# Kernel optimization log

Measured on AMD Instinct MI355X. Metric: run time of the kernel, lower is better.

Reference implementation:

```python
import jax, jax.numpy as jnp
import numpy as np

EPS = 1e-12  # matches NTMNet epsilon


def setup_inputs() -> dict:
    key = jax.random.key(0)
    ks = jax.random.split(key, 12)
    B, L, C, D, H = 64, 16384, 64, 256, 100
    F = D + 1 * C  # inputs concat flattened reading (1 reader)
    def w(k, shape):
        return jax.random.normal(k, shape, dtype=jnp.float32) * 0.05
    return {
        "inputs": w(ks[0], (B, D)),
        "reading": w(ks[1], (B, 1, C)),
        "memory": w(ks[2], (B, L, C)),
        "W1": w(ks[3], (F, H)), "b1": jnp.zeros((H,), jnp.float32),
        "W2": w(ks[4], (H, H)), "b2": jnp.zeros((H,), jnp.float32),
        "Wk_r": w(ks[5], (H, C)), "bk_r": jnp.zeros((C,), jnp.float32),
        "Ws_r": w(ks[6], (H, 1)), "bs_r": jnp.zeros((1,), jnp.float32),
        "Wk_w": w(ks[7], (H, C)), "bk_w": jnp.zeros((C,), jnp.float32),
        "Ws_w": w(ks[8], (H, 1)), "bs_w": jnp.zeros((1,), jnp.float32),
        "We": w(ks[9], (H, C)), "be": jnp.zeros((C,), jnp.float32),
        "Wa": w(ks[10], (H, C)), "ba": jnp.zeros((C,), jnp.float32),
    }


def reference(inputs, reading, memory, W1, b1, W2, b2,
              Wk_r, bk_r, Ws_r, bs_r, Wk_w, bk_w, Ws_w, bs_w,
              We, be, Wa, ba):
    B = inputs.shape[0]
    feat = jnp.concatenate([inputs, reading.reshape(B, -1)], axis=-1)
    h = jnp.tanh(jnp.tanh(feat @ W1 + b1) @ W2 + b2)  # [B,H]

    # memory normalized over the whole (lines, cols) matrix per batch element
    mnorm = jnp.sqrt(jnp.sum(memory * memory, axis=(-2, -1), keepdims=True))
    mem_n = memory / jnp.maximum(mnorm, EPS)  # [B,L,C]

    def addressing(Wk, bk, Ws, bs):
        # content addressing: cosine-sim of key vs memory rows, sharpened softmax
        kvec = h @ Wk + bk  # [B,C] (no activation)
        kvec = kvec / jnp.maximum(jnp.linalg.norm(kvec, axis=1, keepdims=True), EPS)
        s = jax.nn.sigmoid(h @ Ws + bs)  # [B,1] strength
        K = jnp.einsum('blc,bc->bl', mem_n, kvec)  # [B,L]
        return jax.nn.softmax(K * s, axis=-1)  # [B,L]

    # read head
    w_r = addressing(Wk_r, bk_r, Ws_r, bs_r)
    read = jnp.einsum('bl,blc->bc', w_r, memory)  # [B,C]

    # write head: erase then add
    w_w = addressing(Wk_w, bk_w, Ws_w, bs_w)
    e = jax.nn.sigmoid(h @ We + be)  # [B,C]
    a = jax.nn.sigmoid(h @ Wa + ba)  # [B,C]
    ww = w_w[:, :, None]  # [B,L,1]
    new_mem = memory * (1.0 - ww * e[:, None, :]) + ww * a[:, None, :]  # [B,L,C]
    return read, new_mem
```

## Files before the change

### kernel.cpp

```cpp
#include <hip/hip_runtime.h>
#include <math.h>

#define B 64
#define L 16384
#define C 64
#define D 256
#define H 100
#define F 320
#define EPSV 1e-12f

typedef float nfloat4 __attribute__((ext_vector_type(4)));

__device__ inline float waveReduceSum(float v) {
    v += __shfl_xor(v, 32);
    v += __shfl_xor(v, 16);
    v += __shfl_xor(v, 8);
    v += __shfl_xor(v, 4);
    v += __shfl_xor(v, 2);
    v += __shfl_xor(v, 1);
    return v;
}

__global__ __launch_bounds__(128) void head_kernel(
    const float* __restrict__ inputs, const float* __restrict__ reading,
    const float* __restrict__ W1, const float* __restrict__ b1,
    const float* __restrict__ W2, const float* __restrict__ b2,
    const float* __restrict__ Wk_r, const float* __restrict__ bk_r,
    const float* __restrict__ Ws_r, const float* __restrict__ bs_r,
    const float* __restrict__ Wk_w, const float* __restrict__ bk_w,
    const float* __restrict__ Ws_w, const float* __restrict__ bs_w,
    const float* __restrict__ We, const float* __restrict__ be,
    const float* __restrict__ Wa, const float* __restrict__ ba,
    float* __restrict__ kv_r, float* __restrict__ kv_w,
    float* __restrict__ ev, float* __restrict__ av,
    float* __restrict__ s_r, float* __restrict__ s_w)
{
    const int b = blockIdx.x;
    const int t = threadIdx.x;
    __shared__ float feat[F];
    __shared__ float h1[H];
    __shared__ float h2[H];
    __shared__ float kr[C], kw[C], ee[C], aa[C];
    __shared__ float inv_r, inv_w;

    for (int i = t; i < D; i += 128) feat[i] = inputs[b * D + i];
    if (t < C) feat[D + t] = reading[b * C + t];
    __syncthreads();

    if (t < H) {
        float acc = b1[t];
        for (int f = 0; f < F; ++f) acc += feat[f] * W1[f * H + t];
        h1[t] = tanhf(acc);
    }
    __syncthreads();
    if (t < H) {
        float acc = b2[t];
        for (int k = 0; k < H; ++k) acc += h1[k] * W2[k * H + t];
        h2[t] = tanhf(acc);
    }
    __syncthreads();

    if (t < C) {
        float a0 = bk_r[t], a1 = bk_w[t], a2 = be[t], a3 = ba[t];
        for (int j = 0; j < H; ++j) {
            float hv = h2[j];
            a0 += hv * Wk_r[j * C + t];
            a1 += hv * Wk_w[j * C + t];
            a2 += hv * We[j * C + t];
            a3 += hv * Wa[j * C + t];
        }
        kr[t] = a0; kw[t] = a1;
        ee[t] = 1.f / (1.f + expf(-a2));
        aa[t] = 1.f / (1.f + expf(-a3));
    } else if (t == 64 || t == 65) {
        const float* Ws = (t == 64) ? Ws_r : Ws_w;
        float acc = (t == 64) ? bs_r[0] : bs_w[0];
        for (int j = 0; j < H; ++j) acc += h2[j] * Ws[j];
        float s = 1.f / (1.f + expf(-acc));
        if (t == 64) s_r[b] = s; else s_w[b] = s;
    }
    __syncthreads();
    if (t < 64) {
        const float xr = kr[t], xw = kw[t];
        const float nr = waveReduceSum(xr * xr);
        const float nw = waveReduceSum(xw * xw);
        if (t == 0) {
            inv_r = 1.f / fmaxf(sqrtf(nr), EPSV);
            inv_w = 1.f / fmaxf(sqrtf(nw), EPSV);
        }
    }
    __syncthreads();
    if (t < C) {
        kv_r[b * C + t] = kr[t] * inv_r;
        kv_w[b * C + t] = kw[t] * inv_w;
        ev[b * C + t] = ee[t];
        av[b * C + t] = aa[t];
    }
}

__global__ __launch_bounds__(256) void passA_kernel(
    const float* __restrict__ mem,
    const float* __restrict__ kv_r, const float* __restrict__ kv_w,
    float2* __restrict__ dot2,
    float* __restrict__ sumsq)
{
    const int b = blockIdx.y;
    const int t = threadIdx.x;
    const int wave = t >> 6, lane = t & 63;
    const int sub = lane >> 4, m = lane & 15;

    const float4 kr = *(const float4*)(kv_r + b * C + m * 4);
    const float4 kw = *(const float4*)(kv_w + b * C + m * 4);
    const float4* memv = (const float4*)(mem + (size_t)b * L * C);
    float2* d2 = dot2 + (size_t)b * L;

    float lss = 0.f;
    const int row0 = blockIdx.x * 512;
    #pragma unroll 4
    for (int it = 0; it < 32; ++it) {
        const int row = row0 + it * 16 + wave * 4 + sub;
        const float4 v = memv[row * 16 + m];
        float pr = v.x * kr.x + v.y * kr.y + v.z * kr.z + v.w * kr.w;
        float pw = v.x * kw.x + v.y * kw.y + v.z * kw.z + v.w * kw.w;
        lss += v.x * v.x + v.y * v.y + v.z * v.z + v.w * v.w;
        pr += __shfl_xor(pr, 1);
        pw += __shfl_xor(pw, 1);
        float x = (m & 1) ? pw : pr;
        x += __shfl_xor(x, 2);
        x += __shfl_xor(x, 4);
        x += __shfl_xor(x, 8);
        const float y = __shfl_xor(x, 1);
        if (m == 0) d2[row] = make_float2(x, y);
    }
    lss = waveReduceSum(lss);
    __shared__ float wsum[4];
    if (lane == 0) wsum[wave] = lss;
    __syncthreads();
    if (t == 0) atomicAdd(&sumsq[b], wsum[0] + wsum[1] + wsum[2] + wsum[3]);
}

__global__ __launch_bounds__(1024) void stats_kernel(
    const float2* __restrict__ dot2,
    const float* __restrict__ s_r, const float* __restrict__ s_w,
    const float* __restrict__ sumsq,
    float* __restrict__ stats)
{
    const int b = blockIdx.x;
    const int t = threadIdx.x;
    const int wave = t >> 6, lane = t & 63;
    const float invn = 1.f / fmaxf(sqrtf(sumsq[b]), EPSV);
    const float sc_r = s_r[b] * invn;
    const float sc_w = s_w[b] * invn;
    const float2* p = dot2 + (size_t)b * L;

    float2 v[16];
    #pragma unroll
    for (int k = 0; k < 16; ++k) v[k] = p[t + k * 1024];

    float mr = -INFINITY, mw = -INFINITY;
    #pragma unroll
    for (int k = 0; k < 16; ++k) {
        mr = fmaxf(mr, v[k].x * sc_r);
        mw = fmaxf(mw, v[k].y * sc_w);
    }
    #pragma unroll
    for (int off = 32; off; off >>= 1) {
        mr = fmaxf(mr, __shfl_xor(mr, off));
        mw = fmaxf(mw, __shfl_xor(mw, off));
    }
    __shared__ float redr[16], redw[16];
    if (lane == 0) { redr[wave] = mr; redw[wave] = mw; }
    __syncthreads();
    if (t == 0) {
        float a = redr[0], c = redw[0];
        for (int i = 1; i < 16; ++i) { a = fmaxf(a, redr[i]); c = fmaxf(c, redw[i]); }
        redr[0] = a; redw[0] = c;
    }
    __syncthreads();
    const float bmr = redr[0], bmw = redw[0];
    __syncthreads();

    float sr = 0.f, sw = 0.f;
    #pragma unroll
    for (int k = 0; k < 16; ++k) {
        sr += expf(v[k].x * sc_r - bmr);
        sw += expf(v[k].y * sc_w - bmw);
    }
    sr = waveReduceSum(sr);
    sw = waveReduceSum(sw);
    if (lane == 0) { redr[wave] = sr; redw[wave] = sw; }
    __syncthreads();
    if (t == 0) {
        float a = 0.f, c = 0.f;
        for (int i = 0; i < 16; ++i) { a += redr[i]; c += redw[i]; }
        float* st = stats + b * 8;
        st[0] = sc_r; st[1] = bmr; st[2] = 1.f / a;
        st[3] = sc_w; st[4] = bmw; st[5] = 1.f / c;
    }
}

__global__ __launch_bounds__(256) void passB_kernel(
    const float* __restrict__ mem,
    const float2* __restrict__ dot2,
    const float* __restrict__ stats,
    const float* __restrict__ ev, const float* __restrict__ av,
    float* __restrict__ out_read, float* __restrict__ new_mem)
{
    const int b = blockIdx.y;
    const int t = threadIdx.x;
    const int wave = t >> 6, lane = t & 63;
    const int sub = lane >> 4, m = lane & 15;

    const float4 e4 = *(const float4*)(ev + b * C + m * 4);
    const float4 a4 = *(const float4*)(av + b * C + m * 4);
    const float* st = stats + b * 8;
    const float sc_r = st[0], mx_r = st[1], inv_r = st[2];
    const float sc_w = st[3], mx_w = st[4], inv_w = st[5];
    const float4* memv = (const float4*)(mem + (size_t)b * L * C);
    nfloat4* outv = (nfloat4*)(new_mem + (size_t)b * L * C);
    const float2* d2 = dot2 + (size_t)b * L;

    float4 racc = {0.f, 0.f, 0.f, 0.f};
    const int row0 = blockIdx.x * 512;
    #pragma unroll 2
    for (int it = 0; it < 32; ++it) {
        const int row = row0 + it * 16 + wave * 4 + sub;
        const float2 d = d2[row];
        const float wr = expf(d.x * sc_r - mx_r) * inv_r;
        const float ww = expf(d.y * sc_w - mx_w) * inv_w;
        const float4 v = memv[row * 16 + m];
        nfloat4 nm;
        nm.x = v.x * (1.f - ww * e4.x) + ww * a4.x;
        nm.y = v.y * (1.f - ww * e4.y) + ww * a4.y;
        nm.z = v.z * (1.f - ww * e4.z) + ww * a4.z;
        nm.w = v.w * (1.f - ww * e4.w) + ww * a4.w;
        __builtin_nontemporal_store(nm, &outv[row * 16 + m]);
        racc.x += wr * v.x; racc.y += wr * v.y;
        racc.z += wr * v.z; racc.w += wr * v.w;
    }
    racc.x += __shfl_xor(racc.x, 16); racc.x += __shfl_xor(racc.x, 32);
    racc.y += __shfl_xor(racc.y, 16); racc.y += __shfl_xor(racc.y, 32);
    racc.z += __shfl_xor(racc.z, 16); racc.z += __shfl_xor(racc.z, 32);
    racc.w += __shfl_xor(racc.w, 16); racc.w += __shfl_xor(racc.w, 32);
    __shared__ float lds[4][64];
    if (lane < 16) {
        lds[wave][m * 4 + 0] = racc.x;
        lds[wave][m * 4 + 1] = racc.y;
        lds[wave][m * 4 + 2] = racc.z;
        lds[wave][m * 4 + 3] = racc.w;
    }
    __syncthreads();
    if (t < 64) {
        float tot = lds[0][t] + lds[1][t] + lds[2][t] + lds[3][t];
        atomicAdd(&out_read[b * C + t], tot);
    }
}

extern "C" void kernel_launch(void* const* d_in, const int* in_sizes, int n_in,
                              void* d_out, int out_size, void* d_ws, size_t ws_size,
                              hipStream_t stream) {
    const float* inputs  = (const float*)d_in[0];
    const float* reading = (const float*)d_in[1];
    const float* memory  = (const float*)d_in[2];
    const float* W1 = (const float*)d_in[3];
    const float* b1 = (const float*)d_in[4];
    const float* W2 = (const float*)d_in[5];
    const float* b2 = (const float*)d_in[6];
    const float* Wk_r = (const float*)d_in[7];
    const float* bk_r = (const float*)d_in[8];
    const float* Ws_r = (const float*)d_in[9];
    const float* bs_r = (const float*)d_in[10];
    const float* Wk_w = (const float*)d_in[11];
    const float* bk_w = (const float*)d_in[12];
    const float* Ws_w = (const float*)d_in[13];
    const float* bs_w = (const float*)d_in[14];
    const float* We = (const float*)d_in[15];
    const float* be = (const float*)d_in[16];
    const float* Wa = (const float*)d_in[17];
    const float* ba = (const float*)d_in[18];

    float* ws = (float*)d_ws;
    float* kv_r  = ws;
    float* kv_w  = ws + 4096;
    float* ev    = ws + 8192;
    float* av    = ws + 12288;
    float* s_r   = ws + 16384;
    float* s_w   = ws + 16448;
    float* sumsq = ws + 16512;
    float* stats = ws + 16576;
    float* dot2f = ws + 17408;

    float* out = (float*)d_out;
    float* out_read = out;
    float* new_mem  = out + 4096;

    hipMemsetAsync(sumsq, 0, B * sizeof(float), stream);
    hipMemsetAsync(out_read, 0, B * C * sizeof(float), stream);

    head_kernel<<<B, 128, 0, stream>>>(
        inputs, reading, W1, b1, W2, b2, Wk_r, bk_r, Ws_r, bs_r,
        Wk_w, bk_w, Ws_w, bs_w, We, be, Wa, ba,
        kv_r, kv_w, ev, av, s_r, s_w);

    passA_kernel<<<dim3(32, B), 256, 0, stream>>>(
        memory, kv_r, kv_w, (float2*)dot2f, sumsq);

    stats_kernel<<<B, 1024, 0, stream>>>(
        (const float2*)dot2f, s_r, s_w, sumsq, stats);

    passB_kernel<<<dim3(32, B), 256, 0, stream>>>(
        memory, (const float2*)dot2f, stats, ev, av, out_read, new_mem);
}
```

Before: 570.7 us.

## Fuse all four stages into one cooperative persistent kernel with grid syncs

```diff
diff --git a/kernel.cpp b/kernel.cpp
--- a/kernel.cpp
+++ b/kernel.cpp
@@ -1,5 +1,8 @@
 #include <hip/hip_runtime.h>
+#include <hip/hip_cooperative_groups.h>
 #include <math.h>
+
+namespace cg = cooperative_groups;
 
 #define B 64
 #define L 16384
@@ -8,6 +11,8 @@
 #define H 100
 #define F 320
 #define EPSV 1e-12f
+#define MAXBLK 1024
+#define RPB 1024
 
 typedef float nfloat4 __attribute__((ext_vector_type(4)));
 
@@ -19,6 +24,234 @@
     v += __shfl_xor(v, 2);
     v += __shfl_xor(v, 1);
     return v;
+}
+
+__device__ inline void grid_sync_coherent(cg::grid_group& grid) {
+    __threadfence();
+    grid.sync();
+    __threadfence();
+}
+
+__global__ __launch_bounds__(256, 4) void fused_kernel(
+    const float* __restrict__ inputs, const float* __restrict__ reading,
+    const float* __restrict__ mem,
+    const float* __restrict__ W1, const float* __restrict__ b1,
+    const float* __restrict__ W2, const float* __restrict__ b2,
+    const float* __restrict__ Wk_r, const float* __restrict__ bk_r,
+    const float* __restrict__ Ws_r, const float* __restrict__ bs_r,
+    const float* __restrict__ Wk_w, const float* __restrict__ bk_w,
+    const float* __restrict__ Ws_w, const float* __restrict__ bs_w,
+    const float* __restrict__ We, const float* __restrict__ be,
+    const float* __restrict__ Wa, const float* __restrict__ ba,
+    float* __restrict__ kv_r, float* __restrict__ kv_w,
+    float* __restrict__ ev, float* __restrict__ av,
+    float* __restrict__ s_r, float* __restrict__ s_w,
+    float* __restrict__ sumsq, float* __restrict__ stats,
+    float2* __restrict__ dot2,
+    float* __restrict__ out_read, float* __restrict__ new_mem)
+{
+    cg::grid_group grid = cg::this_grid();
+    const int g = blockIdx.x;
+    const int nb = gridDim.x;
+    const int t = threadIdx.x;
+    const int wave = t >> 6, lane = t & 63;
+    const int sub = lane >> 4, m = lane & 15;
+
+    __shared__ float feat[F];
+    __shared__ float h1[H], h2[H];
+    __shared__ float kr_s[C], kw_s[C], ee_s[C], aa_s[C];
+    __shared__ float invs[2];
+    __shared__ float red0[4], red1[4];
+    __shared__ float lds4[4][C];
+
+    for (int u = g; u < 2 * B; u += nb) {
+        if (u < B) {
+            const int b = u;
+            feat[t] = inputs[b * D + t];
+            if (t < C) feat[D + t] = reading[b * C + t];
+            __syncthreads();
+            if (t < H) {
+                float acc = b1[t];
+                for (int f = 0; f < F; ++f) acc += feat[f] * W1[f * H + t];
+                h1[t] = tanhf(acc);
+            }
+            __syncthreads();
+            if (t < H) {
+                float acc = b2[t];
+                for (int k = 0; k < H; ++k) acc += h1[k] * W2[k * H + t];
+                h2[t] = tanhf(acc);
+            }
+            __syncthreads();
+            if (t < C) {
+                float a0 = bk_r[t], a1 = bk_w[t], a2 = be[t], a3 = ba[t];
+                for (int j = 0; j < H; ++j) {
+                    const float hv = h2[j];
+                    a0 += hv * Wk_r[j * C + t];
+                    a1 += hv * Wk_w[j * C + t];
+                    a2 += hv * We[j * C + t];
+                    a3 += hv * Wa[j * C + t];
+                }
+                kr_s[t] = a0; kw_s[t] = a1;
+                ee_s[t] = 1.f / (1.f + expf(-a2));
+                aa_s[t] = 1.f / (1.f + expf(-a3));
+            } else if (t == 64 || t == 65) {
+                const float* Ws = (t == 64) ? Ws_r : Ws_w;
+                float acc = (t == 64) ? bs_r[0] : bs_w[0];
+                for (int j = 0; j < H; ++j) acc += h2[j] * Ws[j];
+                const float s = 1.f / (1.f + expf(-acc));
+                if (t == 64) s_r[b] = s; else s_w[b] = s;
+            }
+            __syncthreads();
+            if (t < 64) {
+                const float xr = kr_s[t], xw = kw_s[t];
+                const float nr = waveReduceSum(xr * xr);
+                const float nw = waveReduceSum(xw * xw);
+                if (t == 0) {
+                    invs[0] = 1.f / fmaxf(sqrtf(nr), EPSV);
+                    invs[1] = 1.f / fmaxf(sqrtf(nw), EPSV);
+                }
+            }
+            __syncthreads();
+            if (t < C) {
+                kv_r[b * C + t] = kr_s[t] * invs[0];
+                kv_w[b * C + t] = kw_s[t] * invs[1];
+                ev[b * C + t] = ee_s[t];
+                av[b * C + t] = aa_s[t];
+            }
+            __syncthreads();
+        } else {
+            const int b = u - B;
+            if (t < C) out_read[b * C + t] = 0.f;
+            if (t == 64) sumsq[b] = 0.f;
+        }
+    }
+    grid_sync_coherent(grid);
+
+    for (int u = g; u < B * 16; u += nb) {
+        const int b = u >> 4;
+        const int chunk = u & 15;
+        const float4 kr = *(const float4*)(kv_r + b * C + m * 4);
+        const float4 kw = *(const float4*)(kv_w + b * C + m * 4);
+        const float4* memv = (const float4*)(mem + (size_t)b * L * C);
+        float2* d2 = dot2 + (size_t)b * L;
+        float lss = 0.f;
+        const int row0 = chunk * RPB;
+        #pragma unroll 4
+        for (int it = 0; it < 64; ++it) {
+            const int row = row0 + it * 16 + wave * 4 + sub;
+            const float4 v = memv[row * 16 + m];
+            float pr = v.x * kr.x + v.y * kr.y + v.z * kr.z + v.w * kr.w;
+            float pw = v.x * kw.x + v.y * kw.y + v.z * kw.z + v.w * kw.w;
+            lss += v.x * v.x + v.y * v.y + v.z * v.z + v.w * v.w;
+            pr += __shfl_xor(pr, 1);
+            pw += __shfl_xor(pw, 1);
+            float x = (m & 1) ? pw : pr;
+            x += __shfl_xor(x, 2);
+            x += __shfl_xor(x, 4);
+            x += __shfl_xor(x, 8);
+            const float y = __shfl_xor(x, 1);
+            if (m == 0) d2[row] = make_float2(x, y);
+        }
+        lss = waveReduceSum(lss);
+        if (lane == 0) red0[wave] = lss;
+        __syncthreads();
+        if (t == 0) atomicAdd(&sumsq[b], red0[0] + red0[1] + red0[2] + red0[3]);
+        __syncthreads();
+    }
+    grid_sync_coherent(grid);
+
+    for (int u = g; u < B; u += nb) {
+        const int b = u;
+        const float invn = 1.f / fmaxf(sqrtf(sumsq[b]), EPSV);
+        const float sc_r = s_r[b] * invn;
+        const float sc_w = s_w[b] * invn;
+        const float2* p = dot2 + (size_t)b * L;
+
+        float mr = -INFINITY, mw = -INFINITY;
+        for (int i = t; i < L; i += 256) {
+            const float2 d = p[i];
+            mr = fmaxf(mr, d.x * sc_r);
+            mw = fmaxf(mw, d.y * sc_w);
+        }
+        #pragma unroll
+        for (int off = 32; off; off >>= 1) {
+            mr = fmaxf(mr, __shfl_xor(mr, off));
+            mw = fmaxf(mw, __shfl_xor(mw, off));
+        }
+        __syncthreads();
+        if (lane == 0) { red0[wave] = mr; red1[wave] = mw; }
+        __syncthreads();
+        const float bmr = fmaxf(fmaxf(red0[0], red0[1]), fmaxf(red0[2], red0[3]));
+        const float bmw = fmaxf(fmaxf(red1[0], red1[1]), fmaxf(red1[2], red1[3]));
+
+        float sr = 0.f, sw = 0.f;
+        for (int i = t; i < L; i += 256) {
+            const float2 d = p[i];
+            sr += expf(d.x * sc_r - bmr);
+            sw += expf(d.y * sc_w - bmw);
+        }
+        sr = waveReduceSum(sr);
+        sw = waveReduceSum(sw);
+        __syncthreads();
+        if (lane == 0) { red0[wave] = sr; red1[wave] = sw; }
+        __syncthreads();
+        if (t == 0) {
+            float* st = stats + b * 8;
+            st[0] = sc_r; st[1] = bmr; st[2] = 1.f / (red0[0] + red0[1] + red0[2] + red0[3]);
+            st[3] = sc_w; st[4] = bmw; st[5] = 1.f / (red1[0] + red1[1] + red1[2] + red1[3]);
+        }
+        __syncthreads();
+    }
+    grid_sync_coherent(grid);
+
+    for (int u = g; u < B * 16; u += nb) {
+        const int b = u >> 4;
+        const int chunk = u & 15;
+        const float4 e4 = *(const float4*)(ev + b * C + m * 4);
+        const float4 a4 = *(const float4*)(av + b * C + m * 4);
+        const float* st = stats + b * 8;
+        const float sc_r = st[0], mx_r = st[1], inv_r = st[2];
+        const float sc_w = st[3], mx_w = st[4], inv_w = st[5];
+        const float4* memv = (const float4*)(mem + (size_t)b * L * C);
+        nfloat4* outv = (nfloat4*)(new_mem + (size_t)b * L * C);
+        const float2* d2 = dot2 + (size_t)b * L;
+
+        float4 racc = {0.f, 0.f, 0.f, 0.f};
+        const int row0 = chunk * RPB;
+        #pragma unroll 2
+        for (int it = 0; it < 64; ++it) {
+            const int row = row0 + it * 16 + wave * 4 + sub;
+            const float2 d = d2[row];
+            const float wr = expf(d.x * sc_r - mx_r) * inv_r;
+            const float ww = expf(d.y * sc_w - mx_w) * inv_w;
+            const float4 v = memv[row * 16 + m];
+            nfloat4 nm;
+            nm.x = v.x * (1.f - ww * e4.x) + ww * a4.x;
+            nm.y = v.y * (1.f - ww * e4.y) + ww * a4.y;
+            nm.z = v.z * (1.f - ww * e4.z) + ww * a4.z;
+            nm.w = v.w * (1.f - ww * e4.w) + ww * a4.w;
+            __builtin_nontemporal_store(nm, &outv[row * 16 + m]);
+            racc.x += wr * v.x; racc.y += wr * v.y;
+            racc.z += wr * v.z; racc.w += wr * v.w;
+        }
+        racc.x += __shfl_xor(racc.x, 16); racc.x += __shfl_xor(racc.x, 32);
+        racc.y += __shfl_xor(racc.y, 16); racc.y += __shfl_xor(racc.y, 32);
+        racc.z += __shfl_xor(racc.z, 16); racc.z += __shfl_xor(racc.z, 32);
+        racc.w += __shfl_xor(racc.w, 16); racc.w += __shfl_xor(racc.w, 32);
+        __syncthreads();
+        if (lane < 16) {
+            lds4[wave][m * 4 + 0] = racc.x;
+            lds4[wave][m * 4 + 1] = racc.y;
+            lds4[wave][m * 4 + 2] = racc.z;
+            lds4[wave][m * 4 + 3] = racc.w;
+        }
+        __syncthreads();
+        if (t < 64) {
+            const float tot = lds4[0][t] + lds4[1][t] + lds4[2][t] + lds4[3][t];
+            atomicAdd(&out_read[b * C + t], tot);
+        }
+        __syncthreads();
+    }
 }
 
 __global__ __launch_bounds__(128) void head_kernel(
@@ -288,14 +521,50 @@
     float* s_w   = ws + 16448;
     float* sumsq = ws + 16512;
     float* stats = ws + 16576;
-    float* dot2f = ws + 17408;
+    float2* dot2 = (float2*)(ws + 17408);
 
     float* out = (float*)d_out;
     float* out_read = out;
     float* new_mem  = out + 4096;
 
-    hipMemsetAsync(sumsq, 0, B * sizeof(float), stream);
-    hipMemsetAsync(out_read, 0, B * C * sizeof(float), stream);
+    static int coop_blocks = -2;
+    if (coop_blocks == -2) {
+        int dev = 0;
+        (void)hipGetDevice(&dev);
+        int supports = 0;
+        (void)hipDeviceGetAttribute(&supports, hipDeviceAttributeCooperativeLaunch, dev);
+        int numCU = 0;
+        (void)hipDeviceGetAttribute(&numCU, hipDeviceAttributeMultiprocessorCount, dev);
+        int perCU = 0;
+        hipError_t oe = hipOccupancyMaxActiveBlocksPerMultiprocessor(
+            &perCU, (const void*)fused_kernel, 256, 0);
+        if (supports && oe == hipSuccess && perCU > 0 && numCU > 0) {
+            long total = (long)perCU * (long)numCU;
+            coop_blocks = (int)(total > MAXBLK ? MAXBLK : total);
+        } else {
+            coop_blocks = -1;
+        }
+    }
+
+    if (coop_blocks > 0) {
+        void* args[] = {
+            (void*)&inputs, (void*)&reading, (void*)&memory,
+            (void*)&W1, (void*)&b1, (void*)&W2, (void*)&b2,
+            (void*)&Wk_r, (void*)&bk_r, (void*)&Ws_r, (void*)&bs_r,
+            (void*)&Wk_w, (void*)&bk_w, (void*)&Ws_w, (void*)&bs_w,
+            (void*)&We, (void*)&be, (void*)&Wa, (void*)&ba,
+            (void*)&kv_r, (void*)&kv_w, (void*)&ev, (void*)&av,
+            (void*)&s_r, (void*)&s_w, (void*)&sumsq, (void*)&stats,
+            (void*)&dot2, (void*)&out_read, (void*)&new_mem
+        };
+        hipError_t err = hipLaunchCooperativeKernel(
+            (void*)fused_kernel, dim3(coop_blocks), dim3(256), args, 0, stream);
+        if (err == hipSuccess) return;
+        coop_blocks = -1;
+    }
+
+    (void)hipMemsetAsync(sumsq, 0, B * sizeof(float), stream);
+    (void)hipMemsetAsync(out_read, 0, B * C * sizeof(float), stream);
 
     head_kernel<<<B, 128, 0, stream>>>(
         inputs, reading, W1, b1, W2, b2, Wk_r, bk_r, Ws_r, bs_r,
@@ -303,11 +572,11 @@
         kv_r, kv_w, ev, av, s_r, s_w);
 
     passA_kernel<<<dim3(32, B), 256, 0, stream>>>(
-        memory, kv_r, kv_w, (float2*)dot2f, sumsq);
+        memory, kv_r, kv_w, dot2, sumsq);
 
     stats_kernel<<<B, 1024, 0, stream>>>(
-        (const float2*)dot2f, s_r, s_w, sumsq, stats);
+        dot2, s_r, s_w, sumsq, stats);
 
     passB_kernel<<<dim3(32, B), 256, 0, stream>>>(
-        memory, (const float2*)dot2f, stats, ev, av, out_read, new_mem);
-}
+        memory, dot2, stats, ev, av, out_read, new_mem);
+}
```

Result: slower. 1.009 ms (+76.9%).

## Drop softmax max pass and dot buffer by recomputing dots across three memory passes

Applied to the files above, without the earlier changes.

```diff
diff --git a/kernel.cpp b/kernel.cpp
--- a/kernel.cpp
+++ b/kernel.cpp
@@ -8,6 +8,8 @@
 #define H 100
 #define F 320
 #define EPSV 1e-12f
+#define CHUNKS 32
+#define RPC 512
 
 typedef float nfloat4 __attribute__((ext_vector_type(4)));
 
@@ -21,8 +23,9 @@
     return v;
 }
 
-__global__ __launch_bounds__(128) void head_kernel(
+__global__ __launch_bounds__(256) void k1_kernel(
     const float* __restrict__ inputs, const float* __restrict__ reading,
+    const float* __restrict__ mem,
     const float* __restrict__ W1, const float* __restrict__ b1,
     const float* __restrict__ W2, const float* __restrict__ b2,
     const float* __restrict__ Wk_r, const float* __restrict__ bk_r,
@@ -33,96 +36,131 @@
     const float* __restrict__ Wa, const float* __restrict__ ba,
     float* __restrict__ kv_r, float* __restrict__ kv_w,
     float* __restrict__ ev, float* __restrict__ av,
-    float* __restrict__ s_r, float* __restrict__ s_w)
+    float* __restrict__ s_r, float* __restrict__ s_w,
+    float* __restrict__ partial_ss)
 {
-    const int b = blockIdx.x;
+    const int g = blockIdx.x;
     const int t = threadIdx.x;
-    __shared__ float feat[F];
-    __shared__ float h1[H];
-    __shared__ float h2[H];
-    __shared__ float kr[C], kw[C], ee[C], aa[C];
-    __shared__ float inv_r, inv_w;
-
-    for (int i = t; i < D; i += 128) feat[i] = inputs[b * D + i];
-    if (t < C) feat[D + t] = reading[b * C + t];
-    __syncthreads();
-
-    if (t < H) {
-        float acc = b1[t];
-        for (int f = 0; f < F; ++f) acc += feat[f] * W1[f * H + t];
-        h1[t] = tanhf(acc);
-    }
-    __syncthreads();
-    if (t < H) {
-        float acc = b2[t];
-        for (int k = 0; k < H; ++k) acc += h1[k] * W2[k * H + t];
-        h2[t] = tanhf(acc);
-    }
-    __syncthreads();
-
-    if (t < C) {
-        float a0 = bk_r[t], a1 = bk_w[t], a2 = be[t], a3 = ba[t];
-        for (int j = 0; j < H; ++j) {
-            float hv = h2[j];
-            a0 += hv * Wk_r[j * C + t];
-            a1 += hv * Wk_w[j * C + t];
-            a2 += hv * We[j * C + t];
-            a3 += hv * Wa[j * C + t];
-        }
-        kr[t] = a0; kw[t] = a1;
-        ee[t] = 1.f / (1.f + expf(-a2));
-        aa[t] = 1.f / (1.f + expf(-a3));
-    } else if (t == 64 || t == 65) {
-        const float* Ws = (t == 64) ? Ws_r : Ws_w;
-        float acc = (t == 64) ? bs_r[0] : bs_w[0];
-        for (int j = 0; j < H; ++j) acc += h2[j] * Ws[j];
-        float s = 1.f / (1.f + expf(-acc));
-        if (t == 64) s_r[b] = s; else s_w[b] = s;
-    }
-    __syncthreads();
-    if (t < 64) {
-        const float xr = kr[t], xw = kw[t];
-        const float nr = waveReduceSum(xr * xr);
-        const float nw = waveReduceSum(xw * xw);
-        if (t == 0) {
-            inv_r = 1.f / fmaxf(sqrtf(nr), EPSV);
-            inv_w = 1.f / fmaxf(sqrtf(nw), EPSV);
-        }
-    }
-    __syncthreads();
-    if (t < C) {
-        kv_r[b * C + t] = kr[t] * inv_r;
-        kv_w[b * C + t] = kw[t] * inv_w;
-        ev[b * C + t] = ee[t];
-        av[b * C + t] = aa[t];
-    }
-}
-
-__global__ __launch_bounds__(256) void passA_kernel(
+
+    if (g < B * CHUNKS) {
+        const int b = g >> 5, chunk = g & 31;
+        const int wave = t >> 6, lane = t & 63;
+        const int sub = lane >> 4, m = lane & 15;
+        const float4* memv = (const float4*)(mem + (size_t)b * L * C);
+        float lss = 0.f;
+        const int row0 = chunk * RPC;
+        #pragma unroll 8
+        for (int it = 0; it < 32; ++it) {
+            const int row = row0 + it * 16 + wave * 4 + sub;
+            const float4 v = memv[row * 16 + m];
+            lss = fmaf(v.x, v.x, fmaf(v.y, v.y, fmaf(v.z, v.z, fmaf(v.w, v.w, lss))));
+        }
+        lss = waveReduceSum(lss);
+        __shared__ float wsum[4];
+        if (lane == 0) wsum[wave] = lss;
+        __syncthreads();
+        if (t == 0) partial_ss[g] = wsum[0] + wsum[1] + wsum[2] + wsum[3];
+    } else {
+        const int b = g - B * CHUNKS;
+        __shared__ float feat[F];
+        __shared__ float h1[H], h2[H];
+        __shared__ float kr_s[C], kw_s[C], ee_s[C], aa_s[C];
+        __shared__ float invs[2];
+
+        feat[t] = inputs[b * D + t];
+        if (t < C) feat[D + t] = reading[b * C + t];
+        __syncthreads();
+        if (t < H) {
+            float acc = b1[t];
+            for (int f = 0; f < F; ++f) acc += feat[f] * W1[f * H + t];
+            h1[t] = tanhf(acc);
+        }
+        __syncthreads();
+        if (t < H) {
+            float acc = b2[t];
+            for (int k = 0; k < H; ++k) acc += h1[k] * W2[k * H + t];
+            h2[t] = tanhf(acc);
+        }
+        __syncthreads();
+        if (t < C) {
+            float a0 = bk_r[t], a1 = bk_w[t], a2 = be[t], a3 = ba[t];
+            for (int j = 0; j < H; ++j) {
+                const float hv = h2[j];
+                a0 += hv * Wk_r[j * C + t];
+                a1 += hv * Wk_w[j * C + t];
+                a2 += hv * We[j * C + t];
+                a3 += hv * Wa[j * C + t];
+            }
+            kr_s[t] = a0; kw_s[t] = a1;
+            ee_s[t] = 1.f / (1.f + expf(-a2));
+            aa_s[t] = 1.f / (1.f + expf(-a3));
+        } else if (t == 64 || t == 65) {
+            const float* Ws = (t == 64) ? Ws_r : Ws_w;
+            float acc = (t == 64) ? bs_r[0] : bs_w[0];
+            for (int j = 0; j < H; ++j) acc += h2[j] * Ws[j];
+            const float s = 1.f / (1.f + expf(-acc));
+            if (t == 64) s_r[b] = s; else s_w[b] = s;
+        }
+        __syncthreads();
+        if (t < 64) {
+            const float xr = kr_s[t], xw = kw_s[t];
+            const float nr = waveReduceSum(xr * xr);
+            const float nw = waveReduceSum(xw * xw);
+            if (t == 0) {
+                invs[0] = 1.f / fmaxf(sqrtf(nr), EPSV);
+                invs[1] = 1.f / fmaxf(sqrtf(nw), EPSV);
+            }
+        }
+        __syncthreads();
+        if (t < C) {
+            kv_r[b * C + t] = kr_s[t] * invs[0];
+            kv_w[b * C + t] = kw_s[t] * invs[1];
+            ev[b * C + t] = ee_s[t];
+            av[b * C + t] = aa_s[t];
+        }
+    }
+}
+
+__global__ __launch_bounds__(256) void k2_kernel(
     const float* __restrict__ mem,
     const float* __restrict__ kv_r, const float* __restrict__ kv_w,
-    float2* __restrict__ dot2,
-    float* __restrict__ sumsq)
+    const float* __restrict__ s_r, const float* __restrict__ s_w,
+    const float* __restrict__ partial_ss,
+    float* __restrict__ partial_S, float* __restrict__ out_read)
 {
     const int b = blockIdx.y;
+    const int chunk = blockIdx.x;
     const int t = threadIdx.x;
     const int wave = t >> 6, lane = t & 63;
     const int sub = lane >> 4, m = lane & 15;
 
+    if (chunk == 0 && t < C) out_read[b * C + t] = 0.f;
+
+    __shared__ float sc_sh[2];
+    if (t < 64) {
+        float p = (t < CHUNKS) ? partial_ss[b * CHUNKS + t] : 0.f;
+        p = waveReduceSum(p);
+        if (t == 0) {
+            const float invn = 1.f / fmaxf(sqrtf(p), EPSV);
+            sc_sh[0] = s_r[b] * invn;
+            sc_sh[1] = s_w[b] * invn;
+        }
+    }
+    __syncthreads();
+    const float sc_r = sc_sh[0], sc_w = sc_sh[1];
+
     const float4 kr = *(const float4*)(kv_r + b * C + m * 4);
     const float4 kw = *(const float4*)(kv_w + b * C + m * 4);
     const float4* memv = (const float4*)(mem + (size_t)b * L * C);
-    float2* d2 = dot2 + (size_t)b * L;
-
-    float lss = 0.f;
-    const int row0 = blockIdx.x * 512;
+
+    float er = 0.f, ew = 0.f;
+    const int row0 = chunk * RPC;
     #pragma unroll 4
     for (int it = 0; it < 32; ++it) {
         const int row = row0 + it * 16 + wave * 4 + sub;
         const float4 v = memv[row * 16 + m];
         float pr = v.x * kr.x + v.y * kr.y + v.z * kr.z + v.w * kr.w;
         float pw = v.x * kw.x + v.y * kw.y + v.z * kw.z + v.w * kw.w;
-        lss += v.x * v.x + v.y * v.y + v.z * v.z + v.w * v.w;
         pr += __shfl_xor(pr, 1);
         pw += __shfl_xor(pw, 1);
         float x = (m & 1) ? pw : pr;
@@ -130,113 +168,100 @@
         x += __shfl_xor(x, 4);
         x += __shfl_xor(x, 8);
         const float y = __shfl_xor(x, 1);
-        if (m == 0) d2[row] = make_float2(x, y);
-    }
-    lss = waveReduceSum(lss);
-    __shared__ float wsum[4];
-    if (lane == 0) wsum[wave] = lss;
-    __syncthreads();
-    if (t == 0) atomicAdd(&sumsq[b], wsum[0] + wsum[1] + wsum[2] + wsum[3]);
-}
-
-__global__ __launch_bounds__(1024) void stats_kernel(
-    const float2* __restrict__ dot2,
+        if (m == 0) {
+            er += expf(x * sc_r);
+            ew += expf(y * sc_w);
+        }
+    }
+    er = waveReduceSum(er);
+    ew = waveReduceSum(ew);
+    __shared__ float wr_sh[4], ww_sh[4];
+    if (lane == 0) { wr_sh[wave] = er; ww_sh[wave] = ew; }
+    __syncthreads();
+    if (t == 0) {
+        float* ps = partial_S + (size_t)(b * CHUNKS + chunk) * 2;
+        ps[0] = wr_sh[0] + wr_sh[1] + wr_sh[2] + wr_sh[3];
+        ps[1] = ww_sh[0] + ww_sh[1] + ww_sh[2] + ww_sh[3];
+    }
+}
+
+__global__ __launch_bounds__(256) void k3_kernel(
+    const float* __restrict__ mem,
+    const float* __restrict__ kv_r, const float* __restrict__ kv_w,
     const float* __restrict__ s_r, const float* __restrict__ s_w,
-    const float* __restrict__ sumsq,
-    float* __restrict__ stats)
-{
-    const int b = blockIdx.x;
-    const int t = threadIdx.x;
-    const int wave = t >> 6, lane = t & 63;
-    const float invn = 1.f / fmaxf(sqrtf(sumsq[b]), EPSV);
-    const float sc_r = s_r[b] * invn;
-    const float sc_w = s_w[b] * invn;
-    const float2* p = dot2 + (size_t)b * L;
-
-    float2 v[16];
-    #pragma unroll
-    for (int k = 0; k < 16; ++k) v[k] = p[t + k * 1024];
-
-    float mr = -INFINITY, mw = -INFINITY;
-    #pragma unroll
-    for (int k = 0; k < 16; ++k) {
-        mr = fmaxf(mr, v[k].x * sc_r);
-        mw = fmaxf(mw, v[k].y * sc_w);
-    }
-    #pragma unroll
-    for (int off = 32; off; off >>= 1) {
-        mr = fmaxf(mr, __shfl_xor(mr, off));
-        mw = fmaxf(mw, __shfl_xor(mw, off));
-    }
-    __shared__ float redr[16], redw[16];
-    if (lane == 0) { redr[wave] = mr; redw[wave] = mw; }
-    __syncthreads();
-    if (t == 0) {
-        float a = redr[0], c = redw[0];
-        for (int i = 1; i < 16; ++i) { a = fmaxf(a, redr[i]); c = fmaxf(c, redw[i]); }
-        redr[0] = a; redw[0] = c;
-    }
-    __syncthreads();
-    const float bmr = redr[0], bmw = redw[0];
-    __syncthreads();
-
-    float sr = 0.f, sw = 0.f;
-    #pragma unroll
-    for (int k = 0; k < 16; ++k) {
-        sr += expf(v[k].x * sc_r - bmr);
-        sw += expf(v[k].y * sc_w - bmw);
-    }
-    sr = waveReduceSum(sr);
-    sw = waveReduceSum(sw);
-    if (lane == 0) { redr[wave] = sr; redw[wave] = sw; }
-    __syncthreads();
-    if (t == 0) {
-        float a = 0.f, c = 0.f;
-        for (int i = 0; i < 16; ++i) { a += redr[i]; c += redw[i]; }
-        float* st = stats + b * 8;
-        st[0] = sc_r; st[1] = bmr; st[2] = 1.f / a;
-        st[3] = sc_w; st[4] = bmw; st[5] = 1.f / c;
-    }
-}
-
-__global__ __launch_bounds__(256) void passB_kernel(
-    const float* __restrict__ mem,
-    const float2* __restrict__ dot2,
-    const float* __restrict__ stats,
+    const float* __restrict__ partial_ss, const float* __restrict__ partial_S,
     const float* __restrict__ ev, const float* __restrict__ av,
     float* __restrict__ out_read, float* __restrict__ new_mem)
 {
     const int b = blockIdx.y;
+    const int chunk = blockIdx.x;
     const int t = threadIdx.x;
     const int wave = t >> 6, lane = t & 63;
     const int sub = lane >> 4, m = lane & 15;
 
+    __shared__ float tmp_sh[3];
+    __shared__ float st_sh[4];
+    if (wave == 0) {
+        float p = (lane < CHUNKS) ? partial_ss[b * CHUNKS + lane] : 0.f;
+        p = waveReduceSum(p);
+        if (lane == 0) tmp_sh[0] = p;
+    } else if (wave == 1) {
+        float p = (lane < CHUNKS) ? partial_S[(size_t)(b * CHUNKS + lane) * 2] : 0.f;
+        p = waveReduceSum(p);
+        if (lane == 0) tmp_sh[1] = p;
+    } else if (wave == 2) {
+        float p = (lane < CHUNKS) ? partial_S[(size_t)(b * CHUNKS + lane) * 2 + 1] : 0.f;
+        p = waveReduceSum(p);
+        if (lane == 0) tmp_sh[2] = p;
+    }
+    __syncthreads();
+    if (t == 0) {
+        const float invn = 1.f / fmaxf(sqrtf(tmp_sh[0]), EPSV);
+        st_sh[0] = s_r[b] * invn;
+        st_sh[1] = s_w[b] * invn;
+        st_sh[2] = 1.f / tmp_sh[1];
+        st_sh[3] = 1.f / tmp_sh[2];
+    }
+    __syncthreads();
+    const float sc_r = st_sh[0], sc_w = st_sh[1];
+    const float inv_r = st_sh[2], inv_w = st_sh[3];
+
+    const float4 kr = *(const float4*)(kv_r + b * C + m * 4);
+    const float4 kw = *(const float4*)(kv_w + b * C + m * 4);
     const float4 e4 = *(const float4*)(ev + b * C + m * 4);
     const float4 a4 = *(const float4*)(av + b * C + m * 4);
-    const float* st = stats + b * 8;
-    const float sc_r = st[0], mx_r = st[1], inv_r = st[2];
-    const float sc_w = st[3], mx_w = st[4], inv_w = st[5];
     const float4* memv = (const float4*)(mem + (size_t)b * L * C);
     nfloat4* outv = (nfloat4*)(new_mem + (size_t)b * L * C);
-    const float2* d2 = dot2 + (size_t)b * L;
 
     float4 racc = {0.f, 0.f, 0.f, 0.f};
-    const int row0 = blockIdx.x * 512;
-    #pragma unroll 2
+    const int row0 = chunk * RPC;
+    #pragma unroll 4
     for (int it = 0; it < 32; ++it) {
         const int row = row0 + it * 16 + wave * 4 + sub;
-        const float2 d = d2[row];
-        const float wr = expf(d.x * sc_r - mx_r) * inv_r;
-        const float ww = expf(d.y * sc_w - mx_w) * inv_w;
         const float4 v = memv[row * 16 + m];
+        float pr = v.x * kr.x + v.y * kr.y + v.z * kr.z + v.w * kr.w;
+        float pw = v.x * kw.x + v.y * kw.y + v.z * kw.z + v.w * kw.w;
+        pr += __shfl_xor(pr, 1);
+        pw += __shfl_xor(pw, 1);
+        float x = (m & 1) ? pw : pr;
+        x += __shfl_xor(x, 2);
+        x += __shfl_xor(x, 4);
+        x += __shfl_xor(x, 8);
+        const float y = __shfl_xor(x, 1);
+        const float dr = (m & 1) ? y : x;
+        const float dw = (m & 1) ? x : y;
+        const float wr = expf(dr * sc_r) * inv_r;
+        const float ww = expf(dw * sc_w) * inv_w;
         nfloat4 nm;
         nm.x = v.x * (1.f - ww * e4.x) + ww * a4.x;
         nm.y = v.y * (1.f - ww * e4.y) + ww * a4.y;
         nm.z = v.z * (1.f - ww * e4.z) + ww * a4.z;
         nm.w = v.w * (1.f - ww * e4.w) + ww * a4.w;
         __builtin_nontemporal_store(nm, &outv[row * 16 + m]);
-        racc.x += wr * v.x; racc.y += wr * v.y;
-        racc.z += wr * v.z; racc.w += wr * v.w;
+        racc.x = fmaf(wr, v.x, racc.x);
+        racc.y = fmaf(wr, v.y, racc.y);
+        racc.z = fmaf(wr, v.z, racc.z);
+        racc.w = fmaf(wr, v.w, racc.w);
     }
     racc.x += __shfl_xor(racc.x, 16); racc.x += __shfl_xor(racc.x, 32);
     racc.y += __shfl_xor(racc.y, 16); racc.y += __shfl_xor(racc.y, 32);
@@ -251,7 +276,7 @@
     }
     __syncthreads();
     if (t < 64) {
-        float tot = lds[0][t] + lds[1][t] + lds[2][t] + lds[3][t];
+        const float tot = lds[0][t] + lds[1][t] + lds[2][t] + lds[3][t];
         atomicAdd(&out_read[b * C + t], tot);
     }
 }
@@ -280,34 +305,29 @@
     const float* ba = (const float*)d_in[18];
 
     float* ws = (float*)d_ws;
-    float* kv_r  = ws;
-    float* kv_w  = ws + 4096;
-    float* ev    = ws + 8192;
-    float* av    = ws + 12288;
-    float* s_r   = ws + 16384;
-    float* s_w   = ws + 16448;
-    float* sumsq = ws + 16512;
-    float* stats = ws + 16576;
-    float* dot2f = ws + 17408;
+    float* kv_r       = ws;
+    float* kv_w       = ws + 4096;
+    float* ev         = ws + 8192;
+    float* av         = ws + 12288;
+    float* s_r        = ws + 16384;
+    float* s_w        = ws + 16448;
+    float* partial_ss = ws + 16512;
+    float* partial_S  = ws + 18560;
 
     float* out = (float*)d_out;
     float* out_read = out;
     float* new_mem  = out + 4096;
 
-    hipMemsetAsync(sumsq, 0, B * sizeof(float), stream);
-    hipMemsetAsync(out_read, 0, B * C * sizeof(float), stream);
-
-    head_kernel<<<B, 128, 0, stream>>>(
-        inputs, reading, W1, b1, W2, b2, Wk_r, bk_r, Ws_r, bs_r,
-        Wk_w, bk_w, Ws_w, bs_w, We, be, Wa, ba,
-        kv_r, kv_w, ev, av, s_r, s_w);
-
-    passA_kernel<<<dim3(32, B), 256, 0, stream>>>(
-        memory, kv_r, kv_w, (float2*)dot2f, sumsq);
-
-    stats_kernel<<<B, 1024, 0, stream>>>(
-        (const float2*)dot2f, s_r, s_w, sumsq, stats);
-
-    passB_kernel<<<dim3(32, B), 256, 0, stream>>>(
-        memory, (const float2*)dot2f, stats, ev, av, out_read, new_mem);
-}
+    k1_kernel<<<B * CHUNKS + B, 256, 0, stream>>>(
+        inputs, reading, memory, W1, b1, W2, b2,
+        Wk_r, bk_r, Ws_r, bs_r, Wk_w, bk_w, Ws_w, bs_w,
+        We, be, Wa, ba,
+        kv_r, kv_w, ev, av, s_r, s_w, partial_ss);
+
+    k2_kernel<<<dim3(CHUNKS, B), 256, 0, stream>>>(
+        memory, kv_r, kv_w, s_r, s_w, partial_ss, partial_S, out_read);
+
+    k3_kernel<<<dim3(CHUNKS, B), 256, 0, stream>>>(
+        memory, kv_r, kv_w, s_r, s_w, partial_ss, partial_S,
+        ev, av, out_read, new_mem);
+}
```

After: 580.1 us. No clear change (+1.7%).
